# Kernel optimization log

Measured on AMD Instinct MI355X. Metric: run time of the kernel, lower is better.

## Reference

```python
import jax, jax.numpy as jnp
import numpy as np

B, T, D, H = 2, 2048, 1024, 16
DH = D // H

def setup_inputs() -> dict:
    key = jax.random.key(0)
    ks = jax.random.split(key, 6)
    s = 0.02
    return {
        "x": jax.random.normal(ks[0], (B, T, D), jnp.float32),
        "Wq": jax.random.normal(ks[1], (D, D), jnp.float32) * s,
        "Wk": jax.random.normal(ks[2], (D, D), jnp.float32) * s,
        "Wv": jax.random.normal(ks[3], (D, D), jnp.float32) * s,
        "Wo": jax.random.normal(ks[4], (D, D), jnp.float32) * s,
        "bo": jnp.zeros((D,), jnp.float32),
    }

def reference(x, Wq, Wk, Wv, Wo, bo):
    Bx, Tx, _ = x.shape
    # project and split heads: [B, H, T, DH]
    q = (x @ Wq).reshape(Bx, Tx, H, DH).transpose(0, 2, 1, 3)
    k = (x @ Wk).reshape(Bx, Tx, H, DH).transpose(0, 2, 1, 3)
    v = (x @ Wv).reshape(Bx, Tx, H, DH).transpose(0, 2, 1, 3)
    scores = jnp.einsum("bhqd,bhkd->bhqk", q, k)  # [B,H,T,T]
    causal = jnp.triu(jnp.ones((Tx, Tx), bool), k=1)  # True above diagonal
    scores = jnp.where(causal, -jnp.inf, scores)
    # original scales AFTER masking (equivalent math)
    w = jax.nn.softmax(scores / jnp.sqrt(jnp.float32(DH)), axis=-1)
    # dropout p=0.0 -> identity
    ctx = jnp.einsum("bhqk,bhkd->bhqd", w, v)
    ctx = ctx.transpose(0, 2, 1, 3).reshape(Bx, Tx, D)
    return ctx @ Wo + bo
```

## Files before the change

### kernel.cpp

```cpp
#include <hip/hip_runtime.h>
#include <hip/hip_bf16.h>


typedef __bf16 bf16x8 __attribute__((ext_vector_type(8)));
typedef __bf16 bf16x4 __attribute__((ext_vector_type(4)));
typedef float  f32x4  __attribute__((ext_vector_type(4)));

#define Bx 2
#define Tx 2048
#define Dx 1024
#define Hx 16
#define DHx 64

__global__ __launch_bounds__(256) void prep(const float* __restrict__ x,
                                            const float* __restrict__ W0,
                                            const float* __restrict__ W1,
                                            const float* __restrict__ W2,
                                            const float* __restrict__ W3,
                                            __bf16* __restrict__ xb,
                                            __bf16* __restrict__ Wt) {
    const int z = blockIdx.z;
    if (z == 0) {
        const int blk = blockIdx.y * 16 + blockIdx.x;
        const float* xp = x + (size_t)blk * 16384;
        __bf16* xo = xb + (size_t)blk * 16384;
#pragma unroll
        for (int i = 0; i < 16; i++) {
            float4 v = *(const float4*)(xp + i * 1024 + threadIdx.x * 4);
            bf16x4 o;
            o[0] = (__bf16)v.x; o[1] = (__bf16)v.y; o[2] = (__bf16)v.z; o[3] = (__bf16)v.w;
            *(bf16x4*)(xo + i * 1024 + threadIdx.x * 4) = o;
        }
        return;
    }
    __shared__ float tile[64][65];
    const float* W = (z == 1) ? W0 : (z == 2) ? W1 : (z == 3) ? W2 : W3;
    __bf16* o = Wt + (size_t)(z - 1) * Dx * Dx;
    int k0 = blockIdx.x * 64, n0 = blockIdx.y * 64;
    int t = threadIdx.x;
    int cc = t & 63, rbase = t >> 6;
#pragma unroll
    for (int i = 0; i < 16; i++) {
        int rr = rbase + i * 4;
        tile[rr][cc] = W[(size_t)(k0 + rr) * Dx + n0 + cc];
    }
    __syncthreads();
#pragma unroll
    for (int i = 0; i < 16; i++) {
        int rr = rbase + i * 4;
        o[(size_t)(n0 + rr) * Dx + k0 + cc] = (__bf16)tile[cc][rr];
    }
}

static __device__ __forceinline__ void gload16(const __bf16* g, __bf16* l) {
    __builtin_amdgcn_global_load_lds((const __attribute__((address_space(1))) void*)g,
                                     (__attribute__((address_space(3))) void*)l, 16, 0, 0);
}

__global__ __launch_bounds__(256, 6) void gemm_qkv(const __bf16* __restrict__ A,
                                                   const __bf16* __restrict__ BT,
                                                   __bf16* __restrict__ Qb,
                                                   __bf16* __restrict__ Kb,
                                                   __bf16* __restrict__ Vt) {
    __shared__ __bf16 As[64 * 32];
    __shared__ __bf16 Bs[128 * 32];
    const int t = threadIdx.x;
    const int lane = t & 63, wave = t >> 6;
    const int lane15 = lane & 15, quad = lane >> 4;
    const int m0 = blockIdx.x * 64, n0 = blockIdx.y * 128;
    const int wm = wave & 1, wn = wave >> 1;

    const int srA = wave * 16 + (lane >> 2), sc = (lane & 3) * 8;
    const int srB = wave * 32 + (lane >> 2);
    const __bf16* Ag = A + (size_t)(m0 + srA) * Dx + sc;
    const __bf16* Bg = BT + (size_t)(n0 + srB) * Dx + sc;
    __bf16* Asl  = As + (wave * 16) * 32;
    __bf16* Bsl0 = Bs + (wave * 32) * 32;
    __bf16* Bsl1 = Bs + (wave * 32 + 16) * 32;

    f32x4 acc[2][4];
#pragma unroll
    for (int i = 0; i < 2; i++)
#pragma unroll
        for (int j = 0; j < 4; j++) acc[i][j] = (f32x4){0.f, 0.f, 0.f, 0.f};

    for (int k0 = 0; k0 < Dx; k0 += 32) {
        gload16(Ag, Asl);
        gload16(Bg, Bsl0);
        gload16(Bg + 16 * Dx, Bsl1);
        Ag += 32; Bg += 32;
        __syncthreads();
        bf16x8 af[2], bf[4];
#pragma unroll
        for (int i = 0; i < 2; i++)
            af[i] = *(const bf16x8*)&As[(wm * 32 + i * 16 + lane15) * 32 + quad * 8];
#pragma unroll
        for (int j = 0; j < 4; j++)
            bf[j] = *(const bf16x8*)&Bs[(wn * 64 + j * 16 + lane15) * 32 + quad * 8];
#pragma unroll
        for (int mt = 0; mt < 2; mt++)
#pragma unroll
            for (int nt = 0; nt < 4; nt++)
                acc[mt][nt] = __builtin_amdgcn_mfma_f32_16x16x32_bf16(af[mt], bf[nt], acc[mt][nt], 0, 0, 0);
        __syncthreads();
    }

    const int z = n0 >> 10;
    if (z < 2) {
        __bf16* outp = z ? Kb : Qb;
        const float scale = z ? 1.0f : 0.125f;
#pragma unroll
        for (int mt = 0; mt < 2; mt++)
#pragma unroll
            for (int nt = 0; nt < 4; nt++) {
                const int cc = (n0 + wn * 64 + nt * 16 + lane15) & 1023;
                const int h = cc >> 6, dh = cc & 63;
#pragma unroll
                for (int r4 = 0; r4 < 4; r4++) {
                    const int row = m0 + wm * 32 + mt * 16 + quad * 4 + r4;
                    const int b = row >> 11, tt = row & 2047;
                    outp[(((size_t)(b * Hx + h) * Tx + tt) << 6) + dh] =
                        (__bf16)(acc[mt][nt][r4] * scale);
                }
            }
    } else {
#pragma unroll
        for (int mt = 0; mt < 2; mt++)
#pragma unroll
            for (int nt = 0; nt < 4; nt++) {
                const int cc = (n0 + wn * 64 + nt * 16 + lane15) & 1023;
                const int h = cc >> 6, dh = cc & 63;
#pragma unroll
                for (int r4 = 0; r4 < 4; r4++) {
                    const int row = m0 + wm * 32 + mt * 16 + quad * 4 + r4;
                    const int b = row >> 11, tt = row & 2047;
                    Vt[((size_t)(b * Hx + h) * DHx + dh) * Tx + tt] = (__bf16)acc[mt][nt][r4];
                }
            }
    }
}

__global__ __launch_bounds__(256, 4) void gemm_out(const __bf16* __restrict__ A,
                                                   const __bf16* __restrict__ BT,
                                                   float* __restrict__ outf,
                                                   const float* __restrict__ bias) {
    __shared__ __bf16 As[64 * 32];
    __shared__ __bf16 Bs[64 * 32];
    const int t = threadIdx.x;
    const int lane = t & 63, wave = t >> 6;
    const int lane15 = lane & 15, quad = lane >> 4;
    const int m0 = blockIdx.x * 64, n0 = blockIdx.y * 64;
    const int wm = wave & 1, wn = wave >> 1;

    const int sr = wave * 16 + (lane >> 2), sc = (lane & 3) * 8;
    const __bf16* Ag = A + (size_t)(m0 + sr) * Dx + sc;
    const __bf16* Bg = BT + (size_t)(n0 + sr) * Dx + sc;
    __bf16* Asl = As + (wave * 16) * 32;
    __bf16* Bsl = Bs + (wave * 16) * 32;

    f32x4 acc[2][2];
#pragma unroll
    for (int i = 0; i < 2; i++)
#pragma unroll
        for (int j = 0; j < 2; j++) acc[i][j] = (f32x4){0.f, 0.f, 0.f, 0.f};

    for (int k0 = 0; k0 < Dx; k0 += 32) {
        gload16(Ag, Asl);
        gload16(Bg, Bsl);
        Ag += 32; Bg += 32;
        __syncthreads();
        bf16x8 af[2], bf[2];
#pragma unroll
        for (int i = 0; i < 2; i++) {
            af[i] = *(const bf16x8*)&As[(wm * 32 + i * 16 + lane15) * 32 + quad * 8];
            bf[i] = *(const bf16x8*)&Bs[(wn * 32 + i * 16 + lane15) * 32 + quad * 8];
        }
#pragma unroll
        for (int mt = 0; mt < 2; mt++)
#pragma unroll
            for (int nt = 0; nt < 2; nt++)
                acc[mt][nt] = __builtin_amdgcn_mfma_f32_16x16x32_bf16(af[mt], bf[nt], acc[mt][nt], 0, 0, 0);
        __syncthreads();
    }

#pragma unroll
    for (int mt = 0; mt < 2; mt++)
#pragma unroll
        for (int nt = 0; nt < 2; nt++) {
            const int col = n0 + wn * 32 + nt * 16 + lane15;
#pragma unroll
            for (int r4 = 0; r4 < 4; r4++) {
                const int row = m0 + wm * 32 + mt * 16 + quad * 4 + r4;
                outf[(size_t)row * Dx + col] = acc[mt][nt][r4] + bias[col];
            }
        }
}

__global__ __launch_bounds__(256) void attn_mfma(const __bf16* __restrict__ Q,
                                                 const __bf16* __restrict__ K,
                                                 const __bf16* __restrict__ Vt,
                                                 __bf16* __restrict__ ctx) {
    __shared__ __bf16 Ks[2][64 * 72];
    __shared__ __bf16 Vs[2][64 * 72];
    __shared__ __bf16 Ps[64 * 80];
    const int t = threadIdx.x;
    const int lane = t & 63, wave = t >> 6;
    const int lane15 = lane & 15, quad = lane >> 4;
    const int h = blockIdx.y, b = blockIdx.z;
    const size_t headoff = ((size_t)(b * Hx + h)) * Tx * DHx;
    const __bf16* Kbase = K + headoff;
    const __bf16* Vbase = Vt + headoff;
    const int sr = t >> 2, sc = (t & 3) * 16;

    for (int pass = 0; pass < 2; pass++) {
        const int chunk = pass ? (31 - blockIdx.x) : blockIdx.x;
        const int q0 = chunk * 64;
        const int ktiles = chunk + 1;
        const int qg = q0 + wave * 16 + quad * 4;

        bf16x8 qf0, qf1;
        {
            const __bf16* Qp = Q + headoff + (size_t)(q0 + wave * 16 + lane15) * 64 + quad * 8;
            qf0 = *(const bf16x8*)Qp;
            qf1 = *(const bf16x8*)(Qp + 32);
        }
        f32x4 o[4];
#pragma unroll
        for (int i = 0; i < 4; i++) o[i] = (f32x4){0.f, 0.f, 0.f, 0.f};
        float lpart[4] = {0.f, 0.f, 0.f, 0.f};

        bf16x8 kpre0, kpre1, vpre0, vpre1;
        {
            const __bf16* Kp = Kbase + (size_t)sr * 64 + sc;
            kpre0 = *(const bf16x8*)Kp; kpre1 = *(const bf16x8*)(Kp + 8);
            const __bf16* Vp = Vbase + (size_t)sr * Tx + sc;
            vpre0 = *(const bf16x8*)Vp; vpre1 = *(const bf16x8*)(Vp + 8);
        }

        for (int kt = 0; kt < ktiles; kt++) {
            const int cur = kt & 1;
            *(bf16x8*)&Ks[cur][sr * 72 + sc] = kpre0;
            *(bf16x8*)&Ks[cur][sr * 72 + sc + 8] = kpre1;
            *(bf16x8*)&Vs[cur][sr * 72 + sc] = vpre0;
            *(bf16x8*)&Vs[cur][sr * 72 + sc + 8] = vpre1;
            if (kt + 1 < ktiles) {
                const __bf16* Kp = Kbase + (size_t)((kt + 1) * 64 + sr) * 64 + sc;
                kpre0 = *(const bf16x8*)Kp; kpre1 = *(const bf16x8*)(Kp + 8);
                const __bf16* Vp = Vbase + (size_t)sr * Tx + (kt + 1) * 64 + sc;
                vpre0 = *(const bf16x8*)Vp; vpre1 = *(const bf16x8*)(Vp + 8);
            }
            __syncthreads();

            f32x4 s[4];
#pragma unroll
            for (int nt = 0; nt < 4; nt++) {
                s[nt] = (f32x4){0.f, 0.f, 0.f, 0.f};
                bf16x8 b0 = *(const bf16x8*)&Ks[cur][(nt * 16 + lane15) * 72 + quad * 8];
                s[nt] = __builtin_amdgcn_mfma_f32_16x16x32_bf16(qf0, b0, s[nt], 0, 0, 0);
                bf16x8 b1 = *(const bf16x8*)&Ks[cur][(nt * 16 + lane15) * 72 + 32 + quad * 8];
                s[nt] = __builtin_amdgcn_mfma_f32_16x16x32_bf16(qf1, b1, s[nt], 0, 0, 0);
            }

            const int kbase = kt * 64;
#pragma unroll
            for (int nt = 0; nt < 4; nt++)
#pragma unroll
                for (int reg = 0; reg < 4; reg++) {
                    float e = __expf(s[nt][reg]);
                    if (kbase + nt * 16 + lane15 > qg + reg) e = 0.f;
                    lpart[reg] += e;
                    Ps[(wave * 16 + quad * 4 + reg) * 80 + nt * 16 + lane15] = (__bf16)e;
                }

            bf16x8 pa0 = *(const bf16x8*)&Ps[(wave * 16 + lane15) * 80 + quad * 8];
            bf16x8 pa1 = *(const bf16x8*)&Ps[(wave * 16 + lane15) * 80 + 32 + quad * 8];
#pragma unroll
            for (int dt = 0; dt < 4; dt++) {
                bf16x8 vb0 = *(const bf16x8*)&Vs[cur][(dt * 16 + lane15) * 72 + quad * 8];
                o[dt] = __builtin_amdgcn_mfma_f32_16x16x32_bf16(pa0, vb0, o[dt], 0, 0, 0);
                bf16x8 vb1 = *(const bf16x8*)&Vs[cur][(dt * 16 + lane15) * 72 + 32 + quad * 8];
                o[dt] = __builtin_amdgcn_mfma_f32_16x16x32_bf16(pa1, vb1, o[dt], 0, 0, 0);
            }
        }

        float inv[4];
#pragma unroll
        for (int reg = 0; reg < 4; reg++) {
            float l = lpart[reg];
#pragma unroll
            for (int off = 1; off < 16; off <<= 1) l += __shfl_xor(l, off);
            inv[reg] = 1.f / l;
        }
#pragma unroll
        for (int dt = 0; dt < 4; dt++)
#pragma unroll
            for (int reg = 0; reg < 4; reg++) {
                int q = q0 + wave * 16 + quad * 4 + reg;
                ctx[(((size_t)(b * Tx + q)) * Hx + h) * 64 + dt * 16 + lane15] =
                    (__bf16)(o[dt][reg] * inv[reg]);
            }
        __syncthreads();
    }
}

extern "C" void kernel_launch(void* const* d_in, const int* in_sizes, int n_in,
                              void* d_out, int out_size, void* d_ws, size_t ws_size,
                              hipStream_t stream) {
    const float* x  = (const float*)d_in[0];
    const float* Wq = (const float*)d_in[1];
    const float* Wk = (const float*)d_in[2];
    const float* Wv = (const float*)d_in[3];
    const float* Wo = (const float*)d_in[4];
    const float* bo = (const float*)d_in[5];
    float* out = (float*)d_out;

    char* ws = (char*)d_ws;
    __bf16* xb  = (__bf16*)(ws + 0);
    __bf16* Wt  = (__bf16*)(ws + (8ull << 20));
    __bf16* Qb  = (__bf16*)(ws + (16ull << 20));
    __bf16* Kb  = (__bf16*)(ws + (24ull << 20));
    __bf16* Vtg = (__bf16*)(ws + (32ull << 20));
    __bf16* ctx = (__bf16*)(ws + (40ull << 20));

    prep<<<dim3(16, 16, 5), 256, 0, stream>>>(x, Wq, Wk, Wv, Wo, xb, Wt);

    gemm_qkv<<<dim3(Bx * Tx / 64, 3 * Dx / 128), 256, 0, stream>>>(xb, Wt, Qb, Kb, Vtg);

    attn_mfma<<<dim3(Tx / 128, Hx, Bx), 256, 0, stream>>>(Qb, Kb, Vtg, ctx);

    gemm_out<<<dim3(Bx * Tx / 64, Dx / 64), 256, 0, stream>>>(ctx, Wt + 3 * (1u << 20), out, bo);
}
```

Baseline: 187.1 us.

## Fuse paired causal query chunks into one K/V sweep and flatten grid

Rather than running two passes per block (a short low chunk, then a long high chunk), each reloading K/V tiles, the attention kernel now makes a single sweep over K/V tiles for the high chunk. The low chunk reuses the same staged tiles while kt <= lo. This roughly halves K/V global loads and removes the second pass's pipeline fill. The grid is also flattened to 512 blocks with batch-head index in the low bits, which changes the scheduling order. The cost is doubled accumulator and Q register state, which may lower occupancy.

```diff
diff --git a/kernel.cpp b/kernel.cpp
--- a/kernel.cpp
+++ b/kernel.cpp
@@ -206,101 +206,137 @@
     const int t = threadIdx.x;
     const int lane = t & 63, wave = t >> 6;
     const int lane15 = lane & 15, quad = lane >> 4;
-    const int h = blockIdx.y, b = blockIdx.z;
+    const int id = blockIdx.x;
+    const int bh = id & 31, p = id >> 5;
+    const int b = bh >> 4, h = bh & 15;
+    const int lo = p, hi = 31 - p;
+    const int ktiles = hi + 1;
     const size_t headoff = ((size_t)(b * Hx + h)) * Tx * DHx;
     const __bf16* Kbase = K + headoff;
     const __bf16* Vbase = Vt + headoff;
     const int sr = t >> 2, sc = (t & 3) * 16;
 
-    for (int pass = 0; pass < 2; pass++) {
-        const int chunk = pass ? (31 - blockIdx.x) : blockIdx.x;
-        const int q0 = chunk * 64;
-        const int ktiles = chunk + 1;
-        const int qg = q0 + wave * 16 + quad * 4;
-
-        bf16x8 qf0, qf1;
+    bf16x8 qh0, qh1, ql0, ql1;
+    {
+        const __bf16* Qp = Q + headoff + (size_t)(hi * 64 + wave * 16 + lane15) * 64 + quad * 8;
+        qh0 = *(const bf16x8*)Qp; qh1 = *(const bf16x8*)(Qp + 32);
+        const __bf16* Qp2 = Q + headoff + (size_t)(lo * 64 + wave * 16 + lane15) * 64 + quad * 8;
+        ql0 = *(const bf16x8*)Qp2; ql1 = *(const bf16x8*)(Qp2 + 32);
+    }
+    f32x4 oh[4], ol[4];
+#pragma unroll
+    for (int i = 0; i < 4; i++) { oh[i] = (f32x4){0.f,0.f,0.f,0.f}; ol[i] = (f32x4){0.f,0.f,0.f,0.f}; }
+    float lh[4] = {0.f,0.f,0.f,0.f}, ll[4] = {0.f,0.f,0.f,0.f};
+    const int qgh = hi * 64 + wave * 16 + quad * 4;
+    const int qgl = lo * 64 + wave * 16 + quad * 4;
+
+    bf16x8 kpre0, kpre1, vpre0, vpre1;
+    {
+        const __bf16* Kp = Kbase + (size_t)sr * 64 + sc;
+        kpre0 = *(const bf16x8*)Kp; kpre1 = *(const bf16x8*)(Kp + 8);
+        const __bf16* Vp = Vbase + (size_t)sr * Tx + sc;
+        vpre0 = *(const bf16x8*)Vp; vpre1 = *(const bf16x8*)(Vp + 8);
+    }
+
+    for (int kt = 0; kt < ktiles; kt++) {
+        const int cur = kt & 1;
+        *(bf16x8*)&Ks[cur][sr * 72 + sc] = kpre0;
+        *(bf16x8*)&Ks[cur][sr * 72 + sc + 8] = kpre1;
+        *(bf16x8*)&Vs[cur][sr * 72 + sc] = vpre0;
+        *(bf16x8*)&Vs[cur][sr * 72 + sc + 8] = vpre1;
+        if (kt + 1 < ktiles) {
+            const __bf16* Kp = Kbase + (size_t)((kt + 1) * 64 + sr) * 64 + sc;
+            kpre0 = *(const bf16x8*)Kp; kpre1 = *(const bf16x8*)(Kp + 8);
+            const __bf16* Vp = Vbase + (size_t)sr * Tx + (kt + 1) * 64 + sc;
+            vpre0 = *(const bf16x8*)Vp; vpre1 = *(const bf16x8*)(Vp + 8);
+        }
+        __syncthreads();
+
+        const int kbase = kt * 64;
+
         {
-            const __bf16* Qp = Q + headoff + (size_t)(q0 + wave * 16 + lane15) * 64 + quad * 8;
-            qf0 = *(const bf16x8*)Qp;
-            qf1 = *(const bf16x8*)(Qp + 32);
-        }
-        f32x4 o[4];
-#pragma unroll
-        for (int i = 0; i < 4; i++) o[i] = (f32x4){0.f, 0.f, 0.f, 0.f};
-        float lpart[4] = {0.f, 0.f, 0.f, 0.f};
-
-        bf16x8 kpre0, kpre1, vpre0, vpre1;
-        {
-            const __bf16* Kp = Kbase + (size_t)sr * 64 + sc;
-            kpre0 = *(const bf16x8*)Kp; kpre1 = *(const bf16x8*)(Kp + 8);
-            const __bf16* Vp = Vbase + (size_t)sr * Tx + sc;
-            vpre0 = *(const bf16x8*)Vp; vpre1 = *(const bf16x8*)(Vp + 8);
-        }
-
-        for (int kt = 0; kt < ktiles; kt++) {
-            const int cur = kt & 1;
-            *(bf16x8*)&Ks[cur][sr * 72 + sc] = kpre0;
-            *(bf16x8*)&Ks[cur][sr * 72 + sc + 8] = kpre1;
-            *(bf16x8*)&Vs[cur][sr * 72 + sc] = vpre0;
-            *(bf16x8*)&Vs[cur][sr * 72 + sc + 8] = vpre1;
-            if (kt + 1 < ktiles) {
-                const __bf16* Kp = Kbase + (size_t)((kt + 1) * 64 + sr) * 64 + sc;
-                kpre0 = *(const bf16x8*)Kp; kpre1 = *(const bf16x8*)(Kp + 8);
-                const __bf16* Vp = Vbase + (size_t)sr * Tx + (kt + 1) * 64 + sc;
-                vpre0 = *(const bf16x8*)Vp; vpre1 = *(const bf16x8*)(Vp + 8);
-            }
-            __syncthreads();
-
             f32x4 s[4];
 #pragma unroll
             for (int nt = 0; nt < 4; nt++) {
                 s[nt] = (f32x4){0.f, 0.f, 0.f, 0.f};
                 bf16x8 b0 = *(const bf16x8*)&Ks[cur][(nt * 16 + lane15) * 72 + quad * 8];
-                s[nt] = __builtin_amdgcn_mfma_f32_16x16x32_bf16(qf0, b0, s[nt], 0, 0, 0);
+                s[nt] = __builtin_amdgcn_mfma_f32_16x16x32_bf16(qh0, b0, s[nt], 0, 0, 0);
                 bf16x8 b1 = *(const bf16x8*)&Ks[cur][(nt * 16 + lane15) * 72 + 32 + quad * 8];
-                s[nt] = __builtin_amdgcn_mfma_f32_16x16x32_bf16(qf1, b1, s[nt], 0, 0, 0);
-            }
-
-            const int kbase = kt * 64;
+                s[nt] = __builtin_amdgcn_mfma_f32_16x16x32_bf16(qh1, b1, s[nt], 0, 0, 0);
+            }
 #pragma unroll
             for (int nt = 0; nt < 4; nt++)
 #pragma unroll
                 for (int reg = 0; reg < 4; reg++) {
                     float e = __expf(s[nt][reg]);
-                    if (kbase + nt * 16 + lane15 > qg + reg) e = 0.f;
-                    lpart[reg] += e;
+                    if (kbase + nt * 16 + lane15 > qgh + reg) e = 0.f;
+                    lh[reg] += e;
                     Ps[(wave * 16 + quad * 4 + reg) * 80 + nt * 16 + lane15] = (__bf16)e;
                 }
-
             bf16x8 pa0 = *(const bf16x8*)&Ps[(wave * 16 + lane15) * 80 + quad * 8];
             bf16x8 pa1 = *(const bf16x8*)&Ps[(wave * 16 + lane15) * 80 + 32 + quad * 8];
 #pragma unroll
             for (int dt = 0; dt < 4; dt++) {
                 bf16x8 vb0 = *(const bf16x8*)&Vs[cur][(dt * 16 + lane15) * 72 + quad * 8];
-                o[dt] = __builtin_amdgcn_mfma_f32_16x16x32_bf16(pa0, vb0, o[dt], 0, 0, 0);
+                oh[dt] = __builtin_amdgcn_mfma_f32_16x16x32_bf16(pa0, vb0, oh[dt], 0, 0, 0);
                 bf16x8 vb1 = *(const bf16x8*)&Vs[cur][(dt * 16 + lane15) * 72 + 32 + quad * 8];
-                o[dt] = __builtin_amdgcn_mfma_f32_16x16x32_bf16(pa1, vb1, o[dt], 0, 0, 0);
-            }
-        }
-
-        float inv[4];
+                oh[dt] = __builtin_amdgcn_mfma_f32_16x16x32_bf16(pa1, vb1, oh[dt], 0, 0, 0);
+            }
+        }
+
+        if (kt <= lo) {
+            f32x4 s[4];
+#pragma unroll
+            for (int nt = 0; nt < 4; nt++) {
+                s[nt] = (f32x4){0.f, 0.f, 0.f, 0.f};
+                bf16x8 b0 = *(const bf16x8*)&Ks[cur][(nt * 16 + lane15) * 72 + quad * 8];
+                s[nt] = __builtin_amdgcn_mfma_f32_16x16x32_bf16(ql0, b0, s[nt], 0, 0, 0);
+                bf16x8 b1 = *(const bf16x8*)&Ks[cur][(nt * 16 + lane15) * 72 + 32 + quad * 8];
+                s[nt] = __builtin_amdgcn_mfma_f32_16x16x32_bf16(ql1, b1, s[nt], 0, 0, 0);
+            }
+#pragma unroll
+            for (int nt = 0; nt < 4; nt++)
+#pragma unroll
+                for (int reg = 0; reg < 4; reg++) {
+                    float e = __expf(s[nt][reg]);
+                    if (kbase + nt * 16 + lane15 > qgl + reg) e = 0.f;
+                    ll[reg] += e;
+                    Ps[(wave * 16 + quad * 4 + reg) * 80 + nt * 16 + lane15] = (__bf16)e;
+                }
+            bf16x8 pa0 = *(const bf16x8*)&Ps[(wave * 16 + lane15) * 80 + quad * 8];
+            bf16x8 pa1 = *(const bf16x8*)&Ps[(wave * 16 + lane15) * 80 + 32 + quad * 8];
+#pragma unroll
+            for (int dt = 0; dt < 4; dt++) {
+                bf16x8 vb0 = *(const bf16x8*)&Vs[cur][(dt * 16 + lane15) * 72 + quad * 8];
+                ol[dt] = __builtin_amdgcn_mfma_f32_16x16x32_bf16(pa0, vb0, ol[dt], 0, 0, 0);
+                bf16x8 vb1 = *(const bf16x8*)&Vs[cur][(dt * 16 + lane15) * 72 + 32 + quad * 8];
+                ol[dt] = __builtin_amdgcn_mfma_f32_16x16x32_bf16(pa1, vb1, ol[dt], 0, 0, 0);
+            }
+        }
+    }
+
+#pragma unroll
+    for (int reg = 0; reg < 4; reg++) {
+        float a = lh[reg], c = ll[reg];
+#pragma unroll
+        for (int off = 1; off < 16; off <<= 1) {
+            a += __shfl_xor(a, off);
+            c += __shfl_xor(c, off);
+        }
+        lh[reg] = 1.f / a;
+        ll[reg] = 1.f / c;
+    }
+#pragma unroll
+    for (int dt = 0; dt < 4; dt++)
 #pragma unroll
         for (int reg = 0; reg < 4; reg++) {
-            float l = lpart[reg];
-#pragma unroll
-            for (int off = 1; off < 16; off <<= 1) l += __shfl_xor(l, off);
-            inv[reg] = 1.f / l;
-        }
-#pragma unroll
-        for (int dt = 0; dt < 4; dt++)
-#pragma unroll
-            for (int reg = 0; reg < 4; reg++) {
-                int q = q0 + wave * 16 + quad * 4 + reg;
-                ctx[(((size_t)(b * Tx + q)) * Hx + h) * 64 + dt * 16 + lane15] =
-                    (__bf16)(o[dt][reg] * inv[reg]);
-            }
-        __syncthreads();
-    }
+            int qh = hi * 64 + wave * 16 + quad * 4 + reg;
+            ctx[(((size_t)(b * Tx + qh)) * Hx + h) * 64 + dt * 16 + lane15] =
+                (__bf16)(oh[dt][reg] * lh[reg]);
+            int ql = lo * 64 + wave * 16 + quad * 4 + reg;
+            ctx[(((size_t)(b * Tx + ql)) * Hx + h) * 64 + dt * 16 + lane15] =
+                (__bf16)(ol[dt][reg] * ll[reg]);
+        }
 }
 
 extern "C" void kernel_launch(void* const* d_in, const int* in_sizes, int n_in,
@@ -326,7 +362,7 @@
 
     gemm_qkv<<<dim3(Bx * Tx / 64, 3 * Dx / 128), 256, 0, stream>>>(xb, Wt, Qb, Kb, Vtg);
 
-    attn_mfma<<<dim3(Tx / 128, Hx, Bx), 256, 0, stream>>>(Qb, Kb, Vtg, ctx);
+    attn_mfma<<<dim3(512), 256, 0, stream>>>(Qb, Kb, Vtg, ctx);
 
     gemm_out<<<dim3(Bx * Tx / 64, Dx / 64), 256, 0, stream>>>(ctx, Wt + 3 * (1u << 20), out, bo);
 }
```

New measurement: 188.0 us. Within noise of the previous version (+0.5%).

## Launch one attention block per query chunk, scheduled longest-first

Applied to the files above, without the earlier changes.

The attention kernel no longer pairs a short and a long causal query chunk inside one block across two passes. It now launches 1024 independent blocks, one per (batch, head, chunk), ordered so the chunks with the most key tiles start first. This is meant to spread the triangular causal work more evenly across CUs. The K/V shared-memory double buffer is collapsed to a single buffer with an extra barrier per tile, which lowers LDS use per block but serialises the store and compute phases more.

```diff
diff --git a/kernel.cpp b/kernel.cpp
--- a/kernel.cpp
+++ b/kernel.cpp
@@ -200,107 +200,105 @@
                                                  const __bf16* __restrict__ K,
                                                  const __bf16* __restrict__ Vt,
                                                  __bf16* __restrict__ ctx) {
-    __shared__ __bf16 Ks[2][64 * 72];
-    __shared__ __bf16 Vs[2][64 * 72];
+    __shared__ __bf16 Ks[64 * 72];
+    __shared__ __bf16 Vs[64 * 72];
     __shared__ __bf16 Ps[64 * 80];
     const int t = threadIdx.x;
     const int lane = t & 63, wave = t >> 6;
     const int lane15 = lane & 15, quad = lane >> 4;
-    const int h = blockIdx.y, b = blockIdx.z;
+    const int id = blockIdx.x;
+    const int bh = id & 31, ord = id >> 5;
+    const int chunk = 31 - ord;
+    const int b = bh >> 4, h = bh & 15;
+    const int ktiles = chunk + 1;
+    const int q0 = chunk * 64;
     const size_t headoff = ((size_t)(b * Hx + h)) * Tx * DHx;
     const __bf16* Kbase = K + headoff;
     const __bf16* Vbase = Vt + headoff;
     const int sr = t >> 2, sc = (t & 3) * 16;
-
-    for (int pass = 0; pass < 2; pass++) {
-        const int chunk = pass ? (31 - blockIdx.x) : blockIdx.x;
-        const int q0 = chunk * 64;
-        const int ktiles = chunk + 1;
-        const int qg = q0 + wave * 16 + quad * 4;
-
-        bf16x8 qf0, qf1;
-        {
-            const __bf16* Qp = Q + headoff + (size_t)(q0 + wave * 16 + lane15) * 64 + quad * 8;
-            qf0 = *(const bf16x8*)Qp;
-            qf1 = *(const bf16x8*)(Qp + 32);
-        }
-        f32x4 o[4];
-#pragma unroll
-        for (int i = 0; i < 4; i++) o[i] = (f32x4){0.f, 0.f, 0.f, 0.f};
-        float lpart[4] = {0.f, 0.f, 0.f, 0.f};
-
-        bf16x8 kpre0, kpre1, vpre0, vpre1;
-        {
-            const __bf16* Kp = Kbase + (size_t)sr * 64 + sc;
+    const int qg = q0 + wave * 16 + quad * 4;
+
+    bf16x8 qf0, qf1;
+    {
+        const __bf16* Qp = Q + headoff + (size_t)(q0 + wave * 16 + lane15) * 64 + quad * 8;
+        qf0 = *(const bf16x8*)Qp;
+        qf1 = *(const bf16x8*)(Qp + 32);
+    }
+    f32x4 o[4];
+#pragma unroll
+    for (int i = 0; i < 4; i++) o[i] = (f32x4){0.f, 0.f, 0.f, 0.f};
+    float lpart[4] = {0.f, 0.f, 0.f, 0.f};
+
+    bf16x8 kpre0, kpre1, vpre0, vpre1;
+    {
+        const __bf16* Kp = Kbase + (size_t)sr * 64 + sc;
+        kpre0 = *(const bf16x8*)Kp; kpre1 = *(const bf16x8*)(Kp + 8);
+        const __bf16* Vp = Vbase + (size_t)sr * Tx + sc;
+        vpre0 = *(const bf16x8*)Vp; vpre1 = *(const bf16x8*)(Vp + 8);
+    }
+
+    for (int kt = 0; kt < ktiles; kt++) {
+        __syncthreads();
+        *(bf16x8*)&Ks[sr * 72 + sc] = kpre0;
+        *(bf16x8*)&Ks[sr * 72 + sc + 8] = kpre1;
+        *(bf16x8*)&Vs[sr * 72 + sc] = vpre0;
+        *(bf16x8*)&Vs[sr * 72 + sc + 8] = vpre1;
+        if (kt + 1 < ktiles) {
+            const __bf16* Kp = Kbase + (size_t)((kt + 1) * 64 + sr) * 64 + sc;
             kpre0 = *(const bf16x8*)Kp; kpre1 = *(const bf16x8*)(Kp + 8);
-            const __bf16* Vp = Vbase + (size_t)sr * Tx + sc;
+            const __bf16* Vp = Vbase + (size_t)sr * Tx + (kt + 1) * 64 + sc;
             vpre0 = *(const bf16x8*)Vp; vpre1 = *(const bf16x8*)(Vp + 8);
         }
-
-        for (int kt = 0; kt < ktiles; kt++) {
-            const int cur = kt & 1;
-            *(bf16x8*)&Ks[cur][sr * 72 + sc] = kpre0;
-            *(bf16x8*)&Ks[cur][sr * 72 + sc + 8] = kpre1;
-            *(bf16x8*)&Vs[cur][sr * 72 + sc] = vpre0;
-            *(bf16x8*)&Vs[cur][sr * 72 + sc + 8] = vpre1;
-            if (kt + 1 < ktiles) {
-                const __bf16* Kp = Kbase + (size_t)((kt + 1) * 64 + sr) * 64 + sc;
-                kpre0 = *(const bf16x8*)Kp; kpre1 = *(const bf16x8*)(Kp + 8);
-                const __bf16* Vp = Vbase + (size_t)sr * Tx + (kt + 1) * 64 + sc;
-                vpre0 = *(const bf16x8*)Vp; vpre1 = *(const bf16x8*)(Vp + 8);
+        __syncthreads();
+
+        f32x4 s[4];
+#pragma unroll
+        for (int nt = 0; nt < 4; nt++) {
+            s[nt] = (f32x4){0.f, 0.f, 0.f, 0.f};
+            bf16x8 b0 = *(const bf16x8*)&Ks[(nt * 16 + lane15) * 72 + quad * 8];
+            s[nt] = __builtin_amdgcn_mfma_f32_16x16x32_bf16(qf0, b0, s[nt], 0, 0, 0);
+            bf16x8 b1 = *(const bf16x8*)&Ks[(nt * 16 + lane15) * 72 + 32 + quad * 8];
+            s[nt] = __builtin_amdgcn_mfma_f32_16x16x32_bf16(qf1, b1, s[nt], 0, 0, 0);
+        }
+
+        const int kbase = kt * 64;
+#pragma unroll
+        for (int nt = 0; nt < 4; nt++)
+#pragma unroll
+            for (int reg = 0; reg < 4; reg++) {
+                float e = __expf(s[nt][reg]);
+                if (kbase + nt * 16 + lane15 > qg + reg) e = 0.f;
+                lpart[reg] += e;
+                Ps[(wave * 16 + quad * 4 + reg) * 80 + nt * 16 + lane15] = (__bf16)e;
             }
-            __syncthreads();
-
-            f32x4 s[4];
-#pragma unroll
-            for (int nt = 0; nt < 4; nt++) {
-                s[nt] = (f32x4){0.f, 0.f, 0.f, 0.f};
-                bf16x8 b0 = *(const bf16x8*)&Ks[cur][(nt * 16 + lane15) * 72 + quad * 8];
-                s[nt] = __builtin_amdgcn_mfma_f32_16x16x32_bf16(qf0, b0, s[nt], 0, 0, 0);
-                bf16x8 b1 = *(const bf16x8*)&Ks[cur][(nt * 16 + lane15) * 72 + 32 + quad * 8];
-                s[nt] = __builtin_amdgcn_mfma_f32_16x16x32_bf16(qf1, b1, s[nt], 0, 0, 0);
-            }
-
-            const int kbase = kt * 64;
-#pragma unroll
-            for (int nt = 0; nt < 4; nt++)
-#pragma unroll
-                for (int reg = 0; reg < 4; reg++) {
-                    float e = __expf(s[nt][reg]);
-                    if (kbase + nt * 16 + lane15 > qg + reg) e = 0.f;
-                    lpart[reg] += e;
-                    Ps[(wave * 16 + quad * 4 + reg) * 80 + nt * 16 + lane15] = (__bf16)e;
-                }
-
-            bf16x8 pa0 = *(const bf16x8*)&Ps[(wave * 16 + lane15) * 80 + quad * 8];
-            bf16x8 pa1 = *(const bf16x8*)&Ps[(wave * 16 + lane15) * 80 + 32 + quad * 8];
-#pragma unroll
-            for (int dt = 0; dt < 4; dt++) {
-                bf16x8 vb0 = *(const bf16x8*)&Vs[cur][(dt * 16 + lane15) * 72 + quad * 8];
-                o[dt] = __builtin_amdgcn_mfma_f32_16x16x32_bf16(pa0, vb0, o[dt], 0, 0, 0);
-                bf16x8 vb1 = *(const bf16x8*)&Vs[cur][(dt * 16 + lane15) * 72 + 32 + quad * 8];
-                o[dt] = __builtin_amdgcn_mfma_f32_16x16x32_bf16(pa1, vb1, o[dt], 0, 0, 0);
-            }
-        }
-
-        float inv[4];
+
+        bf16x8 pa0 = *(const bf16x8*)&Ps[(wave * 16 + lane15) * 80 + quad * 8];
+        bf16x8 pa1 = *(const bf16x8*)&Ps[(wave * 16 + lane15) * 80 + 32 + quad * 8];
+#pragma unroll
+        for (int dt = 0; dt < 4; dt++) {
+            bf16x8 vb0 = *(const bf16x8*)&Vs[(dt * 16 + lane15) * 72 + quad * 8];
+            o[dt] = __builtin_amdgcn_mfma_f32_16x16x32_bf16(pa0, vb0, o[dt], 0, 0, 0);
+            bf16x8 vb1 = *(const bf16x8*)&Vs[(dt * 16 + lane15) * 72 + 32 + quad * 8];
+            o[dt] = __builtin_amdgcn_mfma_f32_16x16x32_bf16(pa1, vb1, o[dt], 0, 0, 0);
+        }
+    }
+
+    float inv[4];
+#pragma unroll
+    for (int reg = 0; reg < 4; reg++) {
+        float l = lpart[reg];
+#pragma unroll
+        for (int off = 1; off < 16; off <<= 1) l += __shfl_xor(l, off);
+        inv[reg] = 1.f / l;
+    }
+#pragma unroll
+    for (int dt = 0; dt < 4; dt++)
 #pragma unroll
         for (int reg = 0; reg < 4; reg++) {
-            float l = lpart[reg];
-#pragma unroll
-            for (int off = 1; off < 16; off <<= 1) l += __shfl_xor(l, off);
-            inv[reg] = 1.f / l;
-        }
-#pragma unroll
-        for (int dt = 0; dt < 4; dt++)
-#pragma unroll
-            for (int reg = 0; reg < 4; reg++) {
-                int q = q0 + wave * 16 + quad * 4 + reg;
-                ctx[(((size_t)(b * Tx + q)) * Hx + h) * 64 + dt * 16 + lane15] =
-                    (__bf16)(o[dt][reg] * inv[reg]);
-            }
-        __syncthreads();
-    }
+            int q = q0 + wave * 16 + quad * 4 + reg;
+            ctx[(((size_t)(b * Tx + q)) * Hx + h) * 64 + dt * 16 + lane15] =
+                (__bf16)(o[dt][reg] * inv[reg]);
+        }
 }
 
 extern "C" void kernel_launch(void* const* d_in, const int* in_sizes, int n_in,
@@ -326,7 +324,7 @@
 
     gemm_qkv<<<dim3(Bx * Tx / 64, 3 * Dx / 128), 256, 0, stream>>>(xb, Wt, Qb, Kb, Vtg);
 
-    attn_mfma<<<dim3(Tx / 128, Hx, Bx), 256, 0, stream>>>(Qb, Kb, Vtg, ctx);
+    attn_mfma<<<dim3(1024), 256, 0, stream>>>(Qb, Kb, Vtg, ctx);
 
     gemm_out<<<dim3(Bx * Tx / 64, Dx / 64), 256, 0, stream>>>(ctx, Wt + 3 * (1u << 20), out, bo);
 }
```

Result: no change. 185.0 us (-1.1%).
